# Kernel optimization log

Hardware: AMD Instinct MI355X
Metric: run time of the kernel (lower is better)

## Reference

```python
import jax, jax.numpy as jnp
import numpy as np

B, L, D, H = 4, 1024, 1024, 8


def setup_inputs() -> dict:
    key = jax.random.key(0)
    ks = jax.random.split(key, 6)
    x = jax.random.normal(ks[0], (B, L, D), dtype=jnp.float32)
    src_mask = jax.random.normal(ks[1], (B * H, L, L), dtype=jnp.float32)
    init = 0.02
    Wq = jax.random.normal(ks[2], (D, D), dtype=jnp.float32) * init
    Wk = jax.random.normal(ks[3], (D, D), dtype=jnp.float32) * init
    Wv = jax.random.normal(ks[4], (D, D), dtype=jnp.float32) * init
    Wp = jax.random.normal(ks[5], (D, D), dtype=jnp.float32) * init
    bp = jnp.zeros((D,), dtype=jnp.float32)
    # torch init: ones*2 with first half set to -2
    gating = jnp.concatenate([jnp.full((H // 2,), -2.0, jnp.float32),
                              jnp.full((H - H // 2,), 2.0, jnp.float32)])
    return {"x": x, "src_mask": src_mask, "Wq": Wq, "Wk": Wk, "Wv": Wv,
            "Wp": Wp, "bp": bp, "gating": gating}


def reference(x, src_mask, Wq, Wk, Wv, Wp, bp, gating):
    b, l, d = x.shape
    h = gating.shape[0]
    dh = d // h
    scale = d ** (-0.5)  # note: full dim_out, as in the original module
    # linear projections then split heads: b t (h d) -> b h t d
    q = (x @ Wq).reshape(b, l, h, dh).transpose(0, 2, 1, 3)
    k = (x @ Wk).reshape(b, l, h, dh).transpose(0, 2, 1, 3)
    v = (x @ Wv).reshape(b, l, h, dh).transpose(0, 2, 1, 3)
    score = jnp.einsum('bhld,bhtd->bhlt', q, k) * scale
    attn = jax.nn.softmax(score, axis=-1)
    g = jax.nn.sigmoid(gating)[None, :, None, None]  # (1,h,1,1)
    mask_sm = jax.nn.softmax(src_mask.reshape(b, h, l, l), axis=-1)
    attn = (1.0 - g) * attn + g * mask_sm
    attn = attn / jnp.sum(attn, axis=-1, keepdims=True)
    out = jnp.einsum('bhlt,bhtd->bhld', attn, v)
    out = out.transpose(0, 2, 1, 3).reshape(b, l, d)
    out = out @ Wp + bp
    return out, attn
```

## Files before the change

kernel.cpp:

```cpp
#include <hip/hip_runtime.h>
#include <hip/hip_bf16.h>

using bf16 = __hip_bfloat16;
typedef __bf16 bf16x8 __attribute__((ext_vector_type(8)));
typedef __bf16 bf16x4 __attribute__((ext_vector_type(4)));
typedef float f32x4 __attribute__((ext_vector_type(4)));

#define AS1C(p) ((const __attribute__((address_space(1))) void*)(p))
#define AS3(p)  ((__attribute__((address_space(3))) void*)(p))

static constexpr int BM = 128, BN = 128, BK = 32;

__global__ __launch_bounds__(256)
void cvt_f32_bf16(const float* __restrict__ in, bf16* __restrict__ out) {
    int i = (blockIdx.x * 256 + threadIdx.x) * 4;
    float4 v = *reinterpret_cast<const float4*>(in + i);
    out[i + 0] = __float2bfloat16(v.x);
    out[i + 1] = __float2bfloat16(v.y);
    out[i + 2] = __float2bfloat16(v.z);
    out[i + 3] = __float2bfloat16(v.w);
}

__global__ __launch_bounds__(1024)
void transpose_w(const float* __restrict__ W, bf16* __restrict__ WT) {
    __shared__ float tile[32][33];
    int bx = blockIdx.x * 32, by = blockIdx.y * 32;
    tile[threadIdx.y][threadIdx.x] = W[(size_t)(by + threadIdx.y) * 1024 + bx + threadIdx.x];
    __syncthreads();
    WT[(size_t)(bx + threadIdx.y) * 1024 + by + threadIdx.x] =
        __float2bfloat16(tile[threadIdx.x][threadIdx.y]);
}

__global__ __launch_bounds__(1024)
void transpose_v(const bf16* __restrict__ V, bf16* __restrict__ VT) {
    __shared__ bf16 tile[32][33];
    const bf16* v = V + (size_t)blockIdx.z * 1024 * 128;
    bf16* vt = VT + (size_t)blockIdx.z * 1024 * 128;
    int l0 = blockIdx.x * 32, d0 = blockIdx.y * 32;
    tile[threadIdx.y][threadIdx.x] = v[(size_t)(l0 + threadIdx.y) * 128 + d0 + threadIdx.x];
    __syncthreads();
    vt[(size_t)(d0 + threadIdx.y) * 1024 + l0 + threadIdx.x] = tile[threadIdx.x][threadIdx.y];
}

template<int MODE>
__global__ __launch_bounds__(256)
void gemm_bf16(const bf16* __restrict__ A, const bf16* __restrict__ Bt,
               float* __restrict__ C, const float* __restrict__ bias,
               int M, int N, int K, int lda, int ldb,
               bf16* __restrict__ Qb, bf16* __restrict__ Kb, bf16* __restrict__ Vb)
{
    __shared__ __align__(16) bf16 As[4 * BM * 8];
    __shared__ __align__(16) bf16 Bs[4 * BN * 8];
    const int t = threadIdx.x;
    const int lane = t & 63;
    const int wid = t >> 6;
    const int wm = wid >> 1, wn = wid & 1;
    const int bm0 = blockIdx.x * BM, bn0 = blockIdx.y * BN;

    f32x4 acc[4][4] = {};
    const int gl = lane >> 4, rl = lane & 15;

    for (int k0 = 0; k0 < K; k0 += BK) {
#pragma unroll
        for (int r = 0; r < 2; ++r) {
            int vt = r * 256 + t;
            int gg = vt >> 7, row = vt & 127;
            __builtin_amdgcn_global_load_lds(
                AS1C(A + (size_t)(bm0 + row) * lda + k0 + gg * 8),
                AS3(&As[(size_t)(r * 256 + (t & ~63)) * 8]), 16, 0, 0);
            __builtin_amdgcn_global_load_lds(
                AS1C(Bt + (size_t)(bn0 + row) * ldb + k0 + gg * 8),
                AS3(&Bs[(size_t)(r * 256 + (t & ~63)) * 8]), 16, 0, 0);
        }
        __syncthreads();
        bf16x8 af[4], bfr[4];
#pragma unroll
        for (int m = 0; m < 4; ++m)
            af[m] = *reinterpret_cast<const bf16x8*>(&As[(size_t)(gl * BM + wm * 64 + m * 16 + rl) * 8]);
#pragma unroll
        for (int n = 0; n < 4; ++n)
            bfr[n] = *reinterpret_cast<const bf16x8*>(&Bs[(size_t)(gl * BN + wn * 64 + n * 16 + rl) * 8]);
#pragma unroll
        for (int m = 0; m < 4; ++m)
#pragma unroll
            for (int n = 0; n < 4; ++n)
                acc[m][n] = __builtin_amdgcn_mfma_f32_16x16x32_bf16(af[m], bfr[n], acc[m][n], 0, 0, 0);
        __syncthreads();
    }

#pragma unroll
    for (int m = 0; m < 4; ++m) {
#pragma unroll
        for (int n = 0; n < 4; ++n) {
#pragma unroll
            for (int i = 0; i < 4; ++i) {
                int gm = bm0 + wm * 64 + m * 16 + gl * 4 + i;
                int gn = bn0 + wn * 64 + n * 16 + rl;
                float v = acc[m][n][i];
                if constexpr (MODE == 0) {
                    int which = gn >> 10, c = gn & 1023;
                    int h = c >> 7, d = c & 127;
                    int b = gm >> 10, l = gm & 1023;
                    bf16* dst = which == 0 ? Qb : (which == 1 ? Kb : Vb);
                    dst[(((size_t)(b * 8 + h) * 1024 + l) << 7) + d] = __float2bfloat16(v);
                } else {
                    C[(size_t)gm * (size_t)N + gn] = v + bias[gn];
                }
            }
        }
    }
}

__global__ __launch_bounds__(512)
void fused_attn(const bf16* __restrict__ Qb, const bf16* __restrict__ Kb,
                const bf16* __restrict__ VTb, const float* __restrict__ mask,
                const float* __restrict__ gating,
                float* __restrict__ attn, bf16* __restrict__ Ob)
{
    constexpr int QB = 32;
    constexpr int SSTR = 1032;
    __shared__ __align__(16) bf16 S[QB * SSTR];
    __shared__ float red0[QB][16];
    __shared__ float red1[QB][16];
    __shared__ float rowmax[QB], rowss[QB], rowsm[QB];

    const int tid  = threadIdx.x;
    const int lane = tid & 63, w = tid >> 6;
    const int rl = lane & 15, gl = lane >> 4;
    const int qb = blockIdx.x, bh = blockIdx.y;
    const int b = bh >> 3, h = bh & 7;
    const int q0 = qb * QB;
    const float g = 1.f / (1.f + __expf(-gating[h]));

    const bf16* Qh  = Qb  + (size_t)bh * 1024 * 128;
    const bf16* Kh  = Kb  + (size_t)bh * 1024 * 128;
    const bf16* VTh = VTb + (size_t)bh * 128 * 1024;
    const float* maskh = mask + (size_t)bh * 1024 * 1024;
    float* attnh = attn + (size_t)bh * 1024 * 1024;

    bf16x8 qf[2][4];
#pragma unroll
    for (int mf = 0; mf < 2; ++mf)
#pragma unroll
        for (int ks = 0; ks < 4; ++ks)
            qf[mf][ks] = *reinterpret_cast<const bf16x8*>(
                Qh + (size_t)(q0 + mf * 16 + rl) * 128 + ks * 32 + gl * 8);

    const int t0 = w * 128;
#pragma unroll 1
    for (int nf = 0; nf < 8; ++nf) {
        const int tb = t0 + nf * 16;
        bf16x8 kf[4];
#pragma unroll
        for (int ks = 0; ks < 4; ++ks)
            kf[ks] = *reinterpret_cast<const bf16x8*>(
                Kh + (size_t)(tb + rl) * 128 + ks * 32 + gl * 8);
        f32x4 acc0 = {}, acc1 = {};
#pragma unroll
        for (int ks = 0; ks < 4; ++ks) {
            acc0 = __builtin_amdgcn_mfma_f32_16x16x32_bf16(qf[0][ks], kf[ks], acc0, 0, 0, 0);
            acc1 = __builtin_amdgcn_mfma_f32_16x16x32_bf16(qf[1][ks], kf[ks], acc1, 0, 0, 0);
        }
#pragma unroll
        for (int i = 0; i < 4; ++i) {
            S[(size_t)(gl * 4 + i) * SSTR + tb + rl]        = __float2bfloat16(acc0[i] * 0.03125f);
            S[(size_t)(16 + gl * 4 + i) * SSTR + tb + rl]   = __float2bfloat16(acc1[i] * 0.03125f);
        }
    }
    __syncthreads();

    const int r  = tid >> 4;
    const int c0 = tid & 15;
    float mx = -1e30f;
#pragma unroll
    for (int j = 0; j < 8; ++j) {
        bf16x8 v = *reinterpret_cast<const bf16x8*>(&S[(size_t)r * SSTR + c0 * 8 + j * 128]);
#pragma unroll
        for (int e = 0; e < 8; ++e) mx = fmaxf(mx, (float)v[e]);
    }
    red0[r][c0] = mx;
    __syncthreads();
    if (tid < 32) {
        float m = red0[tid][0];
#pragma unroll
        for (int k = 1; k < 16; ++k) m = fmaxf(m, red0[tid][k]);
        rowmax[tid] = m;
    }
    __syncthreads();
    mx = rowmax[r];

    float ssum = 0.f, msum = 0.f;
#pragma unroll
    for (int j = 0; j < 8; ++j) {
        bf16x8 v = *reinterpret_cast<const bf16x8*>(&S[(size_t)r * SSTR + c0 * 8 + j * 128]);
#pragma unroll
        for (int e = 0; e < 8; ++e) ssum += __expf((float)v[e] - mx);
    }
    const float* mrow = maskh + (size_t)(q0 + r) * 1024;
#pragma unroll
    for (int j = 0; j < 16; ++j) {
        float4 f = *reinterpret_cast<const float4*>(&mrow[c0 * 4 + j * 64]);
        msum += __expf(f.x) + __expf(f.y) + __expf(f.z) + __expf(f.w);
    }
    red0[r][c0] = ssum; red1[r][c0] = msum;
    __syncthreads();
    if (tid < 32) {
        float a = 0.f, m2 = 0.f;
#pragma unroll
        for (int k = 0; k < 16; ++k) { a += red0[tid][k]; m2 += red1[tid][k]; }
        rowss[tid] = a; rowsm[tid] = m2;
    }
    __syncthreads();
    const float cp = (1.f - g) / rowss[r];
    const float cm = g / rowsm[r];
    float* arow = attnh + (size_t)(q0 + r) * 1024;
#pragma unroll
    for (int j = 0; j < 16; ++j) {
        const int c = c0 * 4 + j * 64;
        float4 f = *reinterpret_cast<const float4*>(&mrow[c]);
        bf16x4 sv = *reinterpret_cast<const bf16x4*>(&S[(size_t)r * SSTR + c]);
        float a0 = cp * __expf((float)sv[0] - mx) + cm * __expf(f.x);
        float a1 = cp * __expf((float)sv[1] - mx) + cm * __expf(f.y);
        float a2 = cp * __expf((float)sv[2] - mx) + cm * __expf(f.z);
        float a3 = cp * __expf((float)sv[3] - mx) + cm * __expf(f.w);
        float4 o; o.x = a0; o.y = a1; o.z = a2; o.w = a3;
        *reinterpret_cast<float4*>(&arow[c]) = o;
        bf16x4 sb; sb[0] = (__bf16)a0; sb[1] = (__bf16)a1; sb[2] = (__bf16)a2; sb[3] = (__bf16)a3;
        *reinterpret_cast<bf16x4*>(&S[(size_t)r * SSTR + c]) = sb;
    }
    __syncthreads();

    const int d0 = w * 16;
    f32x4 oacc0 = {}, oacc1 = {};
    for (int ks = 0; ks < 32; ++ks) {
        bf16x8 vf = *reinterpret_cast<const bf16x8*>(
            VTh + (size_t)(d0 + rl) * 1024 + ks * 32 + gl * 8);
        bf16x8 a0 = *reinterpret_cast<const bf16x8*>(&S[(size_t)(rl)      * SSTR + ks * 32 + gl * 8]);
        bf16x8 a1 = *reinterpret_cast<const bf16x8*>(&S[(size_t)(16 + rl) * SSTR + ks * 32 + gl * 8]);
        oacc0 = __builtin_amdgcn_mfma_f32_16x16x32_bf16(a0, vf, oacc0, 0, 0, 0);
        oacc1 = __builtin_amdgcn_mfma_f32_16x16x32_bf16(a1, vf, oacc1, 0, 0, 0);
    }
    bf16* obrow = Ob + ((size_t)b * 1024 + q0) * 1024 + h * 128;
#pragma unroll
    for (int i = 0; i < 4; ++i) {
        obrow[(size_t)(gl * 4 + i)      * 1024 + d0 + rl] = __float2bfloat16(oacc0[i]);
        obrow[(size_t)(16 + gl * 4 + i) * 1024 + d0 + rl] = __float2bfloat16(oacc1[i]);
    }
}

extern "C" void kernel_launch(void* const* d_in, const int* in_sizes, int n_in,
                              void* d_out, int out_size, void* d_ws, size_t ws_size,
                              hipStream_t stream)
{
    const float* x      = (const float*)d_in[0];
    const float* mask   = (const float*)d_in[1];
    const float* Wq     = (const float*)d_in[2];
    const float* Wk     = (const float*)d_in[3];
    const float* Wv     = (const float*)d_in[4];
    const float* Wp     = (const float*)d_in[5];
    const float* bp     = (const float*)d_in[6];
    const float* gating = (const float*)d_in[7];

    float* out      = (float*)d_out;
    float* attn_out = out + (size_t)4 * 1024 * 1024;

    char* w = (char*)d_ws;
    bf16* xb  = (bf16*)(w);
    bf16* Ob  = (bf16*)(w);
    bf16* WT  = (bf16*)(w + ((size_t)8  << 20));
    bf16* Qb  = (bf16*)(w + ((size_t)16 << 20));
    bf16* Kb  = (bf16*)(w + ((size_t)24 << 20));
    bf16* Vb  = (bf16*)(w + ((size_t)32 << 20));
    bf16* VTb = (bf16*)(w + ((size_t)40 << 20));

    const int ONE_M = 1024 * 1024;

    cvt_f32_bf16<<<4096, 256, 0, stream>>>(x, xb);
    dim3 tb(32, 32), tg(32, 32);
    transpose_w<<<tg, tb, 0, stream>>>(Wq, WT + 0 * ONE_M);
    transpose_w<<<tg, tb, 0, stream>>>(Wk, WT + 1 * ONE_M);
    transpose_w<<<tg, tb, 0, stream>>>(Wv, WT + 2 * ONE_M);
    transpose_w<<<tg, tb, 0, stream>>>(Wp, WT + 3 * ONE_M);
    gemm_bf16<0><<<dim3(32, 24, 1), 256, 0, stream>>>(
        xb, WT, nullptr, nullptr, 4096, 3072, 1024, 1024, 1024, Qb, Kb, Vb);
    transpose_v<<<dim3(32, 4, 32), tb, 0, stream>>>(Vb, VTb);
    fused_attn<<<dim3(32, 32), 512, 0, stream>>>(
        Qb, Kb, VTb, mask, gating, attn_out, Ob);
    gemm_bf16<3><<<dim3(32, 8, 1), 256, 0, stream>>>(
        Ob, WT + 3 * ONE_M, out, bp, 4096, 1024, 1024, 1024, 1024,
        nullptr, nullptr, nullptr);
}
```

Baseline: 457.4 us.

## Prefetch K/V fragments and mask into registers, cache exp scores in LDS

Software-pipelines the K fragment loads in the QK^T loop and the V^T loads in the PV loop, so the next tile is fetched while MFMAs run on the current one. The mask row is read once into registers instead of twice from global memory. The exp of scores is stored back to LDS as bf16, so the final pass no longer recomputes it. Launch bounds now request 4 blocks per SM, which adds register pressure from 16 float4 mask registers plus prefetch buffers and risks spills. Storing exp values in bf16 adds a little rounding error.

Result: faster. 447.4 us (-2.2%).

```diff
diff --git a/kernel.cpp b/kernel.cpp
--- a/kernel.cpp
+++ b/kernel.cpp
@@ -111,7 +111,7 @@
     }
 }
 
-__global__ __launch_bounds__(512)
+__global__ __launch_bounds__(512, 4)
 void fused_attn(const bf16* __restrict__ Qb, const bf16* __restrict__ Kb,
                 const bf16* __restrict__ VTb, const float* __restrict__ mask,
                 const float* __restrict__ gating,
@@ -147,14 +147,20 @@
                 Qh + (size_t)(q0 + mf * 16 + rl) * 128 + ks * 32 + gl * 8);
 
     const int t0 = w * 128;
-#pragma unroll 1
+    bf16x8 kf[4], kn[4];
+#pragma unroll
+    for (int ks = 0; ks < 4; ++ks)
+        kf[ks] = *reinterpret_cast<const bf16x8*>(
+            Kh + (size_t)(t0 + rl) * 128 + ks * 32 + gl * 8);
+#pragma unroll
     for (int nf = 0; nf < 8; ++nf) {
         const int tb = t0 + nf * 16;
-        bf16x8 kf[4];
-#pragma unroll
-        for (int ks = 0; ks < 4; ++ks)
-            kf[ks] = *reinterpret_cast<const bf16x8*>(
-                Kh + (size_t)(tb + rl) * 128 + ks * 32 + gl * 8);
+        if (nf < 7) {
+#pragma unroll
+            for (int ks = 0; ks < 4; ++ks)
+                kn[ks] = *reinterpret_cast<const bf16x8*>(
+                    Kh + (size_t)(tb + 16 + rl) * 128 + ks * 32 + gl * 8);
+        }
         f32x4 acc0 = {}, acc1 = {};
 #pragma unroll
         for (int ks = 0; ks < 4; ++ks) {
@@ -163,14 +169,22 @@
         }
 #pragma unroll
         for (int i = 0; i < 4; ++i) {
-            S[(size_t)(gl * 4 + i) * SSTR + tb + rl]        = __float2bfloat16(acc0[i] * 0.03125f);
-            S[(size_t)(16 + gl * 4 + i) * SSTR + tb + rl]   = __float2bfloat16(acc1[i] * 0.03125f);
-        }
+            S[(size_t)(gl * 4 + i) * SSTR + tb + rl]      = __float2bfloat16(acc0[i] * 0.03125f);
+            S[(size_t)(16 + gl * 4 + i) * SSTR + tb + rl] = __float2bfloat16(acc1[i] * 0.03125f);
+        }
+#pragma unroll
+        for (int ks = 0; ks < 4; ++ks) kf[ks] = kn[ks];
     }
     __syncthreads();
 
     const int r  = tid >> 4;
     const int c0 = tid & 15;
+    float4 mf[16];
+#pragma unroll
+    for (int j = 0; j < 8; ++j) {
+        mf[2 * j]     = *reinterpret_cast<const float4*>(&maskh[(size_t)(q0 + r) * 1024 + c0 * 8 + j * 128]);
+        mf[2 * j + 1] = *reinterpret_cast<const float4*>(&maskh[(size_t)(q0 + r) * 1024 + c0 * 8 + j * 128 + 4]);
+    }
     float mx = -1e30f;
 #pragma unroll
     for (int j = 0; j < 8; ++j) {
@@ -193,14 +207,17 @@
 #pragma unroll
     for (int j = 0; j < 8; ++j) {
         bf16x8 v = *reinterpret_cast<const bf16x8*>(&S[(size_t)r * SSTR + c0 * 8 + j * 128]);
-#pragma unroll
-        for (int e = 0; e < 8; ++e) ssum += __expf((float)v[e] - mx);
-    }
-    const float* mrow = maskh + (size_t)(q0 + r) * 1024;
-#pragma unroll
-    for (int j = 0; j < 16; ++j) {
-        float4 f = *reinterpret_cast<const float4*>(&mrow[c0 * 4 + j * 64]);
-        msum += __expf(f.x) + __expf(f.y) + __expf(f.z) + __expf(f.w);
+        bf16x8 ev;
+#pragma unroll
+        for (int e = 0; e < 8; ++e) {
+            float x = __expf((float)v[e] - mx);
+            ssum += x;
+            ev[e] = (__bf16)x;
+        }
+        *reinterpret_cast<bf16x8*>(&S[(size_t)r * SSTR + c0 * 8 + j * 128]) = ev;
+        const float4 f0 = mf[2 * j], f1 = mf[2 * j + 1];
+        msum += __expf(f0.x) + __expf(f0.y) + __expf(f0.z) + __expf(f0.w)
+              + __expf(f1.x) + __expf(f1.y) + __expf(f1.z) + __expf(f1.w);
     }
     red0[r][c0] = ssum; red1[r][c0] = msum;
     __syncthreads();
@@ -215,30 +232,54 @@
     const float cm = g / rowsm[r];
     float* arow = attnh + (size_t)(q0 + r) * 1024;
 #pragma unroll
-    for (int j = 0; j < 16; ++j) {
-        const int c = c0 * 4 + j * 64;
-        float4 f = *reinterpret_cast<const float4*>(&mrow[c]);
-        bf16x4 sv = *reinterpret_cast<const bf16x4*>(&S[(size_t)r * SSTR + c]);
-        float a0 = cp * __expf((float)sv[0] - mx) + cm * __expf(f.x);
-        float a1 = cp * __expf((float)sv[1] - mx) + cm * __expf(f.y);
-        float a2 = cp * __expf((float)sv[2] - mx) + cm * __expf(f.z);
-        float a3 = cp * __expf((float)sv[3] - mx) + cm * __expf(f.w);
-        float4 o; o.x = a0; o.y = a1; o.z = a2; o.w = a3;
-        *reinterpret_cast<float4*>(&arow[c]) = o;
-        bf16x4 sb; sb[0] = (__bf16)a0; sb[1] = (__bf16)a1; sb[2] = (__bf16)a2; sb[3] = (__bf16)a3;
-        *reinterpret_cast<bf16x4*>(&S[(size_t)r * SSTR + c]) = sb;
-    }
-    __syncthreads();
+    for (int j = 0; j < 8; ++j) {
+        const int c = c0 * 8 + j * 128;
+        bf16x8 ev = *reinterpret_cast<const bf16x8*>(&S[(size_t)r * SSTR + c]);
+        const float4 f0 = mf[2 * j], f1 = mf[2 * j + 1];
+        float a0 = cp * (float)ev[0] + cm * __expf(f0.x);
+        float a1 = cp * (float)ev[1] + cm * __expf(f0.y);
+        float a2 = cp * (float)ev[2] + cm * __expf(f0.z);
+        float a3 = cp * (float)ev[3] + cm * __expf(f0.w);
+        float a4 = cp * (float)ev[4] + cm * __expf(f1.x);
+        float a5 = cp * (float)ev[5] + cm * __expf(f1.y);
+        float a6 = cp * (float)ev[6] + cm * __expf(f1.z);
+        float a7 = cp * (float)ev[7] + cm * __expf(f1.w);
+        float4 o0; o0.x = a0; o0.y = a1; o0.z = a2; o0.w = a3;
+        float4 o1; o1.x = a4; o1.y = a5; o1.z = a6; o1.w = a7;
+        *reinterpret_cast<float4*>(&arow[c])     = o0;
+        *reinterpret_cast<float4*>(&arow[c + 4]) = o1;
+        bf16x8 sb;
+        sb[0] = (__bf16)a0; sb[1] = (__bf16)a1; sb[2] = (__bf16)a2; sb[3] = (__bf16)a3;
+        sb[4] = (__bf16)a4; sb[5] = (__bf16)a5; sb[6] = (__bf16)a6; sb[7] = (__bf16)a7;
+        *reinterpret_cast<bf16x8*>(&S[(size_t)r * SSTR + c]) = sb;
+    }
 
     const int d0 = w * 16;
+    bf16x8 vf[4], vn[4];
+#pragma unroll
+    for (int p = 0; p < 4; ++p)
+        vf[p] = *reinterpret_cast<const bf16x8*>(
+            VTh + (size_t)(d0 + rl) * 1024 + p * 32 + gl * 8);
+    __syncthreads();
     f32x4 oacc0 = {}, oacc1 = {};
-    for (int ks = 0; ks < 32; ++ks) {
-        bf16x8 vf = *reinterpret_cast<const bf16x8*>(
-            VTh + (size_t)(d0 + rl) * 1024 + ks * 32 + gl * 8);
-        bf16x8 a0 = *reinterpret_cast<const bf16x8*>(&S[(size_t)(rl)      * SSTR + ks * 32 + gl * 8]);
-        bf16x8 a1 = *reinterpret_cast<const bf16x8*>(&S[(size_t)(16 + rl) * SSTR + ks * 32 + gl * 8]);
-        oacc0 = __builtin_amdgcn_mfma_f32_16x16x32_bf16(a0, vf, oacc0, 0, 0, 0);
-        oacc1 = __builtin_amdgcn_mfma_f32_16x16x32_bf16(a1, vf, oacc1, 0, 0, 0);
+#pragma unroll
+    for (int kb = 0; kb < 8; ++kb) {
+        if (kb < 7) {
+#pragma unroll
+            for (int p = 0; p < 4; ++p)
+                vn[p] = *reinterpret_cast<const bf16x8*>(
+                    VTh + (size_t)(d0 + rl) * 1024 + ((kb + 1) * 4 + p) * 32 + gl * 8);
+        }
+#pragma unroll
+        for (int p = 0; p < 4; ++p) {
+            const int ks = kb * 4 + p;
+            bf16x8 a0 = *reinterpret_cast<const bf16x8*>(&S[(size_t)(rl)      * SSTR + ks * 32 + gl * 8]);
+            bf16x8 a1 = *reinterpret_cast<const bf16x8*>(&S[(size_t)(16 + rl) * SSTR + ks * 32 + gl * 8]);
+            oacc0 = __builtin_amdgcn_mfma_f32_16x16x32_bf16(a0, vf[p], oacc0, 0, 0, 0);
+            oacc1 = __builtin_amdgcn_mfma_f32_16x16x32_bf16(a1, vf[p], oacc1, 0, 0, 0);
+        }
+#pragma unroll
+        for (int p = 0; p < 4; ++p) vf[p] = vn[p];
     }
     bf16* obrow = Ob + ((size_t)b * 1024 + q0) * 1024 + h * 128;
 #pragma unroll
```

## Shrink attention query block, prefetch K/V fragments, and cache exponentials

Applied to the files above, without the earlier changes.

Halves the query block of the fused attention kernel to 16 rows with 256 threads and doubles the grid, so more blocks fit per CU. The mask is read once at the start: its exponentials are kept in registers as bf16 and summed there, replacing the second global read and the repeated exp. Score exponentials are written back to shared memory so the final pass does no exp. K and V^T fragments are software-prefetched one step ahead. Storing the exponentials as bf16 before the weighted sum costs accuracy in the attention output, and the 16 bf16x4 registers per thread raise register pressure.

New measurement: 486.7 us. 1.06x slower.

```diff
diff --git a/kernel.cpp b/kernel.cpp
--- a/kernel.cpp
+++ b/kernel.cpp
@@ -111,13 +111,13 @@
     }
 }
 
-__global__ __launch_bounds__(512)
+__global__ __launch_bounds__(256, 4)
 void fused_attn(const bf16* __restrict__ Qb, const bf16* __restrict__ Kb,
                 const bf16* __restrict__ VTb, const float* __restrict__ mask,
                 const float* __restrict__ gating,
                 float* __restrict__ attn, bf16* __restrict__ Ob)
 {
-    constexpr int QB = 32;
+    constexpr int QB = 16;
     constexpr int SSTR = 1032;
     __shared__ __align__(16) bf16 S[QB * SSTR];
     __shared__ float red0[QB][16];
@@ -138,39 +138,53 @@
     const float* maskh = mask + (size_t)bh * 1024 * 1024;
     float* attnh = attn + (size_t)bh * 1024 * 1024;
 
-    bf16x8 qf[2][4];
-#pragma unroll
-    for (int mf = 0; mf < 2; ++mf)
-#pragma unroll
-        for (int ks = 0; ks < 4; ++ks)
-            qf[mf][ks] = *reinterpret_cast<const bf16x8*>(
-                Qh + (size_t)(q0 + mf * 16 + rl) * 128 + ks * 32 + gl * 8);
-
-    const int t0 = w * 128;
-#pragma unroll 1
-    for (int nf = 0; nf < 8; ++nf) {
-        const int tb = t0 + nf * 16;
-        bf16x8 kf[4];
-#pragma unroll
-        for (int ks = 0; ks < 4; ++ks)
-            kf[ks] = *reinterpret_cast<const bf16x8*>(
-                Kh + (size_t)(tb + rl) * 128 + ks * 32 + gl * 8);
-        f32x4 acc0 = {}, acc1 = {};
-#pragma unroll
-        for (int ks = 0; ks < 4; ++ks) {
-            acc0 = __builtin_amdgcn_mfma_f32_16x16x32_bf16(qf[0][ks], kf[ks], acc0, 0, 0, 0);
-            acc1 = __builtin_amdgcn_mfma_f32_16x16x32_bf16(qf[1][ks], kf[ks], acc1, 0, 0, 0);
-        }
-#pragma unroll
-        for (int i = 0; i < 4; ++i) {
-            S[(size_t)(gl * 4 + i) * SSTR + tb + rl]        = __float2bfloat16(acc0[i] * 0.03125f);
-            S[(size_t)(16 + gl * 4 + i) * SSTR + tb + rl]   = __float2bfloat16(acc1[i] * 0.03125f);
-        }
-    }
-    __syncthreads();
-
     const int r  = tid >> 4;
     const int c0 = tid & 15;
+    float msum = 0.f;
+    bf16x4 em[16];
+#pragma unroll
+    for (int j = 0; j < 16; ++j) {
+        float4 f = *reinterpret_cast<const float4*>(
+            &maskh[(size_t)(q0 + r) * 1024 + c0 * 4 + j * 64]);
+        float e0 = __expf(f.x), e1 = __expf(f.y), e2 = __expf(f.z), e3 = __expf(f.w);
+        msum += e0 + e1 + e2 + e3;
+        bf16x4 e; e[0] = (__bf16)e0; e[1] = (__bf16)e1; e[2] = (__bf16)e2; e[3] = (__bf16)e3;
+        em[j] = e;
+    }
+
+    bf16x8 qf[4];
+#pragma unroll
+    for (int ks = 0; ks < 4; ++ks)
+        qf[ks] = *reinterpret_cast<const bf16x8*>(
+            Qh + (size_t)(q0 + rl) * 128 + ks * 32 + gl * 8);
+
+    const int t0 = w * 256;
+    bf16x8 kf[4], kn[4];
+#pragma unroll
+    for (int ks = 0; ks < 4; ++ks)
+        kf[ks] = *reinterpret_cast<const bf16x8*>(
+            Kh + (size_t)(t0 + rl) * 128 + ks * 32 + gl * 8);
+#pragma unroll
+    for (int nf = 0; nf < 16; ++nf) {
+        const int tb = t0 + nf * 16;
+        if (nf < 15) {
+#pragma unroll
+            for (int ks = 0; ks < 4; ++ks)
+                kn[ks] = *reinterpret_cast<const bf16x8*>(
+                    Kh + (size_t)(tb + 16 + rl) * 128 + ks * 32 + gl * 8);
+        }
+        f32x4 acc = {};
+#pragma unroll
+        for (int ks = 0; ks < 4; ++ks)
+            acc = __builtin_amdgcn_mfma_f32_16x16x32_bf16(qf[ks], kf[ks], acc, 0, 0, 0);
+#pragma unroll
+        for (int i = 0; i < 4; ++i)
+            S[(size_t)(gl * 4 + i) * SSTR + tb + rl] = __float2bfloat16(acc[i] * 0.03125f);
+#pragma unroll
+        for (int ks = 0; ks < 4; ++ks) kf[ks] = kn[ks];
+    }
+    __syncthreads();
+
     float mx = -1e30f;
 #pragma unroll
     for (int j = 0; j < 8; ++j) {
@@ -180,7 +194,7 @@
     }
     red0[r][c0] = mx;
     __syncthreads();
-    if (tid < 32) {
+    if (tid < 16) {
         float m = red0[tid][0];
 #pragma unroll
         for (int k = 1; k < 16; ++k) m = fmaxf(m, red0[tid][k]);
@@ -189,22 +203,22 @@
     __syncthreads();
     mx = rowmax[r];
 
-    float ssum = 0.f, msum = 0.f;
+    float ssum = 0.f;
 #pragma unroll
     for (int j = 0; j < 8; ++j) {
         bf16x8 v = *reinterpret_cast<const bf16x8*>(&S[(size_t)r * SSTR + c0 * 8 + j * 128]);
-#pragma unroll
-        for (int e = 0; e < 8; ++e) ssum += __expf((float)v[e] - mx);
-    }
-    const float* mrow = maskh + (size_t)(q0 + r) * 1024;
-#pragma unroll
-    for (int j = 0; j < 16; ++j) {
-        float4 f = *reinterpret_cast<const float4*>(&mrow[c0 * 4 + j * 64]);
-        msum += __expf(f.x) + __expf(f.y) + __expf(f.z) + __expf(f.w);
+        bf16x8 ev;
+#pragma unroll
+        for (int e = 0; e < 8; ++e) {
+            float x = __expf((float)v[e] - mx);
+            ssum += x;
+            ev[e] = (__bf16)x;
+        }
+        *reinterpret_cast<bf16x8*>(&S[(size_t)r * SSTR + c0 * 8 + j * 128]) = ev;
     }
     red0[r][c0] = ssum; red1[r][c0] = msum;
     __syncthreads();
-    if (tid < 32) {
+    if (tid < 16) {
         float a = 0.f, m2 = 0.f;
 #pragma unroll
         for (int k = 0; k < 16; ++k) { a += red0[tid][k]; m2 += red1[tid][k]; }
@@ -217,34 +231,42 @@
 #pragma unroll
     for (int j = 0; j < 16; ++j) {
         const int c = c0 * 4 + j * 64;
-        float4 f = *reinterpret_cast<const float4*>(&mrow[c]);
-        bf16x4 sv = *reinterpret_cast<const bf16x4*>(&S[(size_t)r * SSTR + c]);
-        float a0 = cp * __expf((float)sv[0] - mx) + cm * __expf(f.x);
-        float a1 = cp * __expf((float)sv[1] - mx) + cm * __expf(f.y);
-        float a2 = cp * __expf((float)sv[2] - mx) + cm * __expf(f.z);
-        float a3 = cp * __expf((float)sv[3] - mx) + cm * __expf(f.w);
+        bf16x4 ev = *reinterpret_cast<const bf16x4*>(&S[(size_t)r * SSTR + c]);
+        bf16x4 e = em[j];
+        float a0 = cp * (float)ev[0] + cm * (float)e[0];
+        float a1 = cp * (float)ev[1] + cm * (float)e[1];
+        float a2 = cp * (float)ev[2] + cm * (float)e[2];
+        float a3 = cp * (float)ev[3] + cm * (float)e[3];
         float4 o; o.x = a0; o.y = a1; o.z = a2; o.w = a3;
         *reinterpret_cast<float4*>(&arow[c]) = o;
         bf16x4 sb; sb[0] = (__bf16)a0; sb[1] = (__bf16)a1; sb[2] = (__bf16)a2; sb[3] = (__bf16)a3;
         *reinterpret_cast<bf16x4*>(&S[(size_t)r * SSTR + c]) = sb;
     }
-    __syncthreads();
-
-    const int d0 = w * 16;
-    f32x4 oacc0 = {}, oacc1 = {};
+
+    const int d0 = w * 32;
+    bf16x8 vfA, vfB, vnA, vnB;
+    vfA = *reinterpret_cast<const bf16x8*>(VTh + (size_t)(d0 + rl)      * 1024 + gl * 8);
+    vfB = *reinterpret_cast<const bf16x8*>(VTh + (size_t)(d0 + 16 + rl) * 1024 + gl * 8);
+    __syncthreads();
+    f32x4 oaccA = {}, oaccB = {};
+#pragma unroll
     for (int ks = 0; ks < 32; ++ks) {
-        bf16x8 vf = *reinterpret_cast<const bf16x8*>(
-            VTh + (size_t)(d0 + rl) * 1024 + ks * 32 + gl * 8);
-        bf16x8 a0 = *reinterpret_cast<const bf16x8*>(&S[(size_t)(rl)      * SSTR + ks * 32 + gl * 8]);
-        bf16x8 a1 = *reinterpret_cast<const bf16x8*>(&S[(size_t)(16 + rl) * SSTR + ks * 32 + gl * 8]);
-        oacc0 = __builtin_amdgcn_mfma_f32_16x16x32_bf16(a0, vf, oacc0, 0, 0, 0);
-        oacc1 = __builtin_amdgcn_mfma_f32_16x16x32_bf16(a1, vf, oacc1, 0, 0, 0);
+        if (ks < 31) {
+            vnA = *reinterpret_cast<const bf16x8*>(
+                VTh + (size_t)(d0 + rl)      * 1024 + (ks + 1) * 32 + gl * 8);
+            vnB = *reinterpret_cast<const bf16x8*>(
+                VTh + (size_t)(d0 + 16 + rl) * 1024 + (ks + 1) * 32 + gl * 8);
+        }
+        bf16x8 a = *reinterpret_cast<const bf16x8*>(&S[(size_t)rl * SSTR + ks * 32 + gl * 8]);
+        oaccA = __builtin_amdgcn_mfma_f32_16x16x32_bf16(a, vfA, oaccA, 0, 0, 0);
+        oaccB = __builtin_amdgcn_mfma_f32_16x16x32_bf16(a, vfB, oaccB, 0, 0, 0);
+        vfA = vnA; vfB = vnB;
     }
     bf16* obrow = Ob + ((size_t)b * 1024 + q0) * 1024 + h * 128;
 #pragma unroll
     for (int i = 0; i < 4; ++i) {
-        obrow[(size_t)(gl * 4 + i)      * 1024 + d0 + rl] = __float2bfloat16(oacc0[i]);
-        obrow[(size_t)(16 + gl * 4 + i) * 1024 + d0 + rl] = __float2bfloat16(oacc1[i]);
+        obrow[(size_t)(gl * 4 + i) * 1024 + d0 + rl]      = __float2bfloat16(oaccA[i]);
+        obrow[(size_t)(gl * 4 + i) * 1024 + d0 + 16 + rl] = __float2bfloat16(oaccB[i]);
     }
 }
 
@@ -284,7 +306,7 @@
     gemm_bf16<0><<<dim3(32, 24, 1), 256, 0, stream>>>(
         xb, WT, nullptr, nullptr, 4096, 3072, 1024, 1024, 1024, Qb, Kb, Vb);
     transpose_v<<<dim3(32, 4, 32), tb, 0, stream>>>(Vb, VTb);
-    fused_attn<<<dim3(32, 32), 512, 0, stream>>>(
+    fused_attn<<<dim3(64, 32), 256, 0, stream>>>(
         Qb, Kb, VTb, mask, gating, attn_out, Ob);
     gemm_bf16<3><<<dim3(32, 8, 1), 256, 0, stream>>>(
         Ob, WT + 3 * ONE_M, out, bp, 4096, 1024, 1024, 1024, 1024,
```
